# Kernel tuning notes

Measured on AMD Instinct MI355X. Metric: run time of the kernel, lower is better.

Reference implementation:

```python
import jax, jax.numpy as jnp
import numpy as np

TEMPERATURE = 0.01  # clamped min is 0.01, so constant temp stays 0.01
MASK_VAL = -10000.0


def setup_inputs() -> dict:
    key = jax.random.key(0)
    k1, k2 = jax.random.split(key)
    B, C, D = 512, 16, 128
    ts_features = jax.random.normal(k1, (B, C, D), dtype=jnp.float32)
    note_features = jax.random.normal(k2, (B, C, D), dtype=jnp.float32)
    return {"ts_features": ts_features, "note_features": note_features}


def reference(ts_features, note_features):
    B, C, D = ts_features.shape
    N = B * C
    ts = ts_features.reshape(N, D)
    nt = note_features.reshape(N, D)

    # sim[i, j] = <ts_i, nt_j>
    sim = jnp.einsum('id,jd->ij', ts, nt)

    # block-diagonal mask: within each CxC block, off-diagonal -> -10000, diagonal kept
    idx = jnp.arange(N)
    blk = idx // C
    same_block = blk[:, None] == blk[None, :]
    is_diag = idx[:, None] == idx[None, :]
    sim_new = jnp.where(same_block & ~is_diag, jnp.asarray(MASK_VAL, sim.dtype), sim)

    logits = sim_new / TEMPERATURE
    # cross entropy with labels = arange(N), both directions
    lsm_r = jax.nn.log_softmax(logits, axis=-1)
    lsm_c = jax.nn.log_softmax(logits.T, axis=-1)
    diag_ids = (idx, idx)
    ce_r = -jnp.mean(lsm_r[diag_ids])
    ce_c = -jnp.mean(lsm_c[diag_ids])
    total_loss = (ce_r + ce_c) / 2

    # nan/inf -> 0 as in the original
    total_loss = jnp.where(jnp.isnan(total_loss) | jnp.isinf(total_loss),
                           jnp.asarray(0.0, total_loss.dtype), total_loss)
    return total_loss
```

## Files before the change

### kernel.cpp

```cpp
#include <hip/hip_runtime.h>
#include <stdint.h>

#define NROWS 8192
#define DDIM  128
#define PPART 8
#define BROWS 256
#define NITER 32
#define LOG2E_X100 144.26950408889634f
#define LN2F       0.6931471805599453f

typedef __bf16 bf16x8 __attribute__((ext_vector_type(8)));
typedef float  f32x4  __attribute__((ext_vector_type(4)));

__device__ __forceinline__ unsigned short f2bf_rne(float f) {
    union { float f; uint32_t u; } v; v.f = f;
    uint32_t r = (v.u + 0x7FFFu + ((v.u >> 16) & 1u)) >> 16;
    return (unsigned short)r;
}

__device__ __forceinline__ void async16(const unsigned short* g, unsigned char* l) {
    __builtin_amdgcn_global_load_lds(
        (const __attribute__((address_space(1))) unsigned int*)g,
        (__attribute__((address_space(3))) unsigned int*)l, 16, 0, 0);
}

__global__ void convert_kernel(const float* __restrict__ ts, const float* __restrict__ nt,
                               unsigned short* __restrict__ ts_bf,
                               unsigned short* __restrict__ nt_bf,
                               float* __restrict__ acc, int* __restrict__ ticket) {
    const int nvec = (NROWS * DDIM) / 4;
    int tid = blockIdx.x * blockDim.x + threadIdx.x;
    bool isNT = tid >= nvec;
    int i = isNT ? (tid - nvec) : tid;
    const float4 v = ((const float4*)(isNT ? nt : ts))[i];
    float sc = isNT ? 1.0f : LOG2E_X100;
    ushort4 o;
    o.x = f2bf_rne(v.x * sc); o.y = f2bf_rne(v.y * sc);
    o.z = f2bf_rne(v.z * sc); o.w = f2bf_rne(v.w * sc);
    ((ushort4*)(isNT ? nt_bf : ts_bf))[i] = o;
    if (tid == 0) { *acc = 0.0f; *ticket = 0; }
}

__device__ __forceinline__ void dma_pair(const unsigned short* gbase, unsigned char* lds, int lane) {
#pragma unroll
    for (int u = 0; u < 8; ++u) {
        int r  = u * 4 + (lane >> 4);
        int ch = (lane & 15) ^ (r & 7);
        async16(gbase + r * 128 + ch * 8, lds + u * 1024);
    }
}

__global__ __launch_bounds__(512, 4) void rowstats_kernel(
        const unsigned short* __restrict__ ts_bf,
        const unsigned short* __restrict__ nt_bf,
        float* __restrict__ pm, float* __restrict__ ps, float* __restrict__ pd) {
    __shared__ unsigned char smem[2 * 8192];

    const int lane = threadIdx.x & 63;
    const int wv   = threadIdx.x >> 6;
    const int c    = lane & 15;
    const int quad = lane >> 4;
    const int bx   = blockIdx.x;
    const int part = blockIdx.y;
    const int dir  = blockIdx.z;
    const int rows0 = bx * BROWS + wv * 32;

    const unsigned short* A = dir ? nt_bf : ts_bf;
    const unsigned short* B = dir ? ts_bf : nt_bf;

    bf16x8 a[2][4];
#pragma unroll
    for (int s = 0; s < 2; ++s) {
        const unsigned short* abase = A + (rows0 + s * 16 + c) * DDIM + quad * 8;
#pragma unroll
        for (int kc = 0; kc < 4; ++kc)
            a[s][kc] = *(const bf16x8*)(abase + kc * 32);
    }

    float m[2][4], ss[2][4], dg[2][4];
#pragma unroll
    for (int s = 0; s < 2; ++s)
#pragma unroll
        for (int r = 0; r < 4; ++r) { m[r? (r):(r)][0] = m[s][r]; }
#pragma unroll
    for (int s = 0; s < 2; ++s)
#pragma unroll
        for (int r = 0; r < 4; ++r) { m[s][r] = -INFINITY; ss[s][r] = 0.0f; dg[s][r] = 0.0f; }

    const bool havePart = (part == (bx >> 2));
    const int  diag_t   = ((bx & 3) << 3) + wv;

    const unsigned short* bwalk = B + (part * (NROWS / PPART)) * DDIM;

    if (wv == 0) dma_pair(bwalk, smem, lane);
    __syncthreads();

    const int ldsoff0 = c * 256 + (((0 * 4) + quad) ^ (c & 7)) * 16;

    for (int t = 0; t < NITER; ++t) {
        if (wv == 0 && t + 1 < NITER)
            dma_pair(bwalk + (t + 1) * 32 * DDIM, smem + ((t + 1) & 1) * 8192, lane);

        const unsigned char* buf = smem + (t & 1) * 8192;

        f32x4 aA0 = {0,0,0,0}, aA1 = {0,0,0,0}, aB0 = {0,0,0,0}, aB1 = {0,0,0,0};
#pragma unroll
        for (int kc = 0; kc < 4; ++kc) {
            const int sw = ((kc * 4 + quad) ^ (c & 7)) * 16;
            bf16x8 bA = *(const bf16x8*)(buf + c * 256 + sw);
            bf16x8 bB = *(const bf16x8*)(buf + (16 + c) * 256 + sw);
            aA0 = __builtin_amdgcn_mfma_f32_16x16x32_bf16(a[0][kc], bA, aA0, 0, 0, 0);
            aA1 = __builtin_amdgcn_mfma_f32_16x16x32_bf16(a[1][kc], bA, aA1, 0, 0, 0);
            aB0 = __builtin_amdgcn_mfma_f32_16x16x32_bf16(a[0][kc], bB, aB0, 0, 0, 0);
            aB1 = __builtin_amdgcn_mfma_f32_16x16x32_bf16(a[1][kc], bB, aB1, 0, 0, 0);
        }

        const bool pd_ = havePart && (t == diag_t);
#pragma unroll
        for (int s = 0; s < 2; ++s) {
#pragma unroll
            for (int r = 0; r < 4; ++r) {
                float xA = s ? aA1[r] : aA0[r];
                float xB = s ? aB1[r] : aB0[r];
                if (pd_) {
                    bool onDiag = (c == quad * 4 + r);
                    if (s == 0) { if (onDiag) dg[0][r] += xA; xA = onDiag ? xA : -1.0e30f; }
                    else        { if (onDiag) dg[1][r] += xB; xB = onDiag ? xB : -1.0e30f; }
                }
                float mn = fmaxf(fmaxf(m[s][r], xA), xB);
                ss[s][r] = ss[s][r] * __builtin_amdgcn_exp2f(m[s][r] - mn)
                         + __builtin_amdgcn_exp2f(xA - mn)
                         + __builtin_amdgcn_exp2f(xB - mn);
                m[s][r] = mn;
            }
        }
        __syncthreads();
    }

#pragma unroll
    for (int s = 0; s < 2; ++s) {
#pragma unroll
        for (int r = 0; r < 4; ++r) {
            float mm = m[s][r], sv = ss[s][r], dd = dg[s][r];
#pragma unroll
            for (int off = 1; off < 16; off <<= 1) {
                float m2 = __shfl_xor(mm, off, 64);
                float s2 = __shfl_xor(sv, off, 64);
                float d2 = __shfl_xor(dd, off, 64);
                float mn = fmaxf(mm, m2);
                sv = sv * __builtin_amdgcn_exp2f(mm - mn) + s2 * __builtin_amdgcn_exp2f(m2 - mn);
                mm = mn;
                dd += d2;
            }
            if (c == 0) {
                int row = rows0 + s * 16 + quad * 4 + r;
                int idx = (dir * NROWS + row) * PPART + part;
                pm[idx] = mm; ps[idx] = sv; pd[idx] = dd;
            }
        }
    }
}

__global__ void merge_kernel(const float* __restrict__ pm, const float* __restrict__ ps,
                             const float* __restrict__ pd, float* __restrict__ acc,
                             int* __restrict__ ticket, float* __restrict__ out) {
    int tid = blockIdx.x * blockDim.x + threadIdx.x;
    const float* pmr = pm + tid * PPART;
    const float* psr = ps + tid * PPART;
    const float* pdr = pd + tid * PPART;
    float mt = -INFINITY;
#pragma unroll
    for (int p = 0; p < PPART; ++p) mt = fmaxf(mt, pmr[p]);
    float st = 0.0f, dt = 0.0f;
#pragma unroll
    for (int p = 0; p < PPART; ++p) {
        st += psr[p] * __builtin_amdgcn_exp2f(pmr[p] - mt);
        dt += pdr[p];
    }
    float lsm = dt - mt - __builtin_amdgcn_logf(st);

    float v = lsm;
#pragma unroll
    for (int off = 32; off; off >>= 1) v += __shfl_down(v, off, 64);
    __shared__ float wsum[4];
    if ((threadIdx.x & 63) == 0) wsum[threadIdx.x >> 6] = v;
    __syncthreads();
    if (threadIdx.x == 0) {
        atomicAdd(acc, wsum[0] + wsum[1] + wsum[2] + wsum[3]);
        __threadfence();
        int old = atomicAdd(ticket, 1);
        if (old == (int)gridDim.x - 1) {
            __threadfence();
            float tot = atomicAdd(acc, 0.0f);
            float t = -(tot * LN2F) / (2.0f * NROWS);
            if (!isfinite(t)) t = 0.0f;
            out[0] = t;
        }
    }
}

extern "C" void kernel_launch(void* const* d_in, const int* in_sizes, int n_in,
                              void* d_out, int out_size, void* d_ws, size_t ws_size,
                              hipStream_t stream) {
    const float* ts = (const float*)d_in[0];
    const float* nt = (const float*)d_in[1];
    float* out = (float*)d_out;

    unsigned short* ts_bf = (unsigned short*)d_ws;
    unsigned short* nt_bf = ts_bf + NROWS * DDIM;
    float* pm = (float*)(nt_bf + NROWS * DDIM);
    float* ps = pm + 2 * NROWS * PPART;
    float* pd = ps + 2 * NROWS * PPART;
    float* acc = pd + 2 * NROWS * PPART;
    int* ticket = (int*)(acc + 1);

    convert_kernel<<<2048, 256, 0, stream>>>(ts, nt, ts_bf, nt_bf, acc, ticket);
    rowstats_kernel<<<dim3(NROWS / BROWS, PPART, 2), 512, 0, stream>>>(ts_bf, nt_bf, pm, ps, pd);
    merge_kernel<<<(2 * NROWS) / 256, 256, 0, stream>>>(pm, ps, pd, acc, ticket, out);
}
```

Baseline: 117.5 us.

## Widen B tiles to 64 rows, spread DMA over all waves, simplify reductions

Result: faster. 110.0 us (-6.4%).

```diff
diff --git a/kernel.cpp b/kernel.cpp
--- a/kernel.cpp
+++ b/kernel.cpp
@@ -5,7 +5,7 @@
 #define DDIM  128
 #define PPART 8
 #define BROWS 256
-#define NITER 32
+#define NITER 16
 #define LOG2E_X100 144.26950408889634f
 #define LN2F       0.6931471805599453f
 
@@ -41,12 +41,14 @@
     if (tid == 0) { *acc = 0.0f; *ticket = 0; }
 }
 
-__device__ __forceinline__ void dma_pair(const unsigned short* gbase, unsigned char* lds, int lane) {
-#pragma unroll
-    for (int u = 0; u < 8; ++u) {
-        int r  = u * 4 + (lane >> 4);
+__device__ __forceinline__ void dma_stage(const unsigned short* g, unsigned char* l,
+                                          int lane, int wv) {
+#pragma unroll
+    for (int k = 0; k < 2; ++k) {
+        int u = wv * 2 + k;
+        int r = u * 4 + (lane >> 4);
         int ch = (lane & 15) ^ (r & 7);
-        async16(gbase + r * 128 + ch * 8, lds + u * 1024);
+        async16(g + r * 128 + ch * 8, l + u * 1024);
     }
 }
 
@@ -54,7 +56,7 @@
         const unsigned short* __restrict__ ts_bf,
         const unsigned short* __restrict__ nt_bf,
         float* __restrict__ pm, float* __restrict__ ps, float* __restrict__ pd) {
-    __shared__ unsigned char smem[2 * 8192];
+    __shared__ unsigned char smem[2 * 16384];
 
     const int lane = threadIdx.x & 63;
     const int wv   = threadIdx.x >> 6;
@@ -81,56 +83,68 @@
 #pragma unroll
     for (int s = 0; s < 2; ++s)
 #pragma unroll
-        for (int r = 0; r < 4; ++r) { m[r? (r):(r)][0] = m[s][r]; }
-#pragma unroll
-    for (int s = 0; s < 2; ++s)
-#pragma unroll
         for (int r = 0; r < 4; ++r) { m[s][r] = -INFINITY; ss[s][r] = 0.0f; dg[s][r] = 0.0f; }
 
     const bool havePart = (part == (bx >> 2));
-    const int  diag_t   = ((bx & 3) << 3) + wv;
-
-    const unsigned short* bwalk = B + (part * (NROWS / PPART)) * DDIM;
-
-    if (wv == 0) dma_pair(bwalk, smem, lane);
+    const int  t_d = (bx & 3) * 4 + (wv >> 1);
+    const int  l0  = (wv & 1) * 2;
+
+    const unsigned short* bwalk = B + part * (NROWS / PPART) * DDIM;
+
+    dma_stage(bwalk, smem, lane, wv);
     __syncthreads();
 
-    const int ldsoff0 = c * 256 + (((0 * 4) + quad) ^ (c & 7)) * 16;
-
     for (int t = 0; t < NITER; ++t) {
-        if (wv == 0 && t + 1 < NITER)
-            dma_pair(bwalk + (t + 1) * 32 * DDIM, smem + ((t + 1) & 1) * 8192, lane);
-
-        const unsigned char* buf = smem + (t & 1) * 8192;
-
-        f32x4 aA0 = {0,0,0,0}, aA1 = {0,0,0,0}, aB0 = {0,0,0,0}, aB1 = {0,0,0,0};
+        if (t + 1 < NITER)
+            dma_stage(bwalk + (t + 1) * 64 * DDIM, smem + ((t + 1) & 1) * 16384, lane, wv);
+
+        const unsigned char* buf = smem + (t & 1) * 16384;
+
+        f32x4 acc[4][2];
+#pragma unroll
+        for (int l = 0; l < 4; ++l)
+#pragma unroll
+            for (int s = 0; s < 2; ++s) acc[l][s] = (f32x4){0.f, 0.f, 0.f, 0.f};
+
 #pragma unroll
         for (int kc = 0; kc < 4; ++kc) {
             const int sw = ((kc * 4 + quad) ^ (c & 7)) * 16;
-            bf16x8 bA = *(const bf16x8*)(buf + c * 256 + sw);
-            bf16x8 bB = *(const bf16x8*)(buf + (16 + c) * 256 + sw);
-            aA0 = __builtin_amdgcn_mfma_f32_16x16x32_bf16(a[0][kc], bA, aA0, 0, 0, 0);
-            aA1 = __builtin_amdgcn_mfma_f32_16x16x32_bf16(a[1][kc], bA, aA1, 0, 0, 0);
-            aB0 = __builtin_amdgcn_mfma_f32_16x16x32_bf16(a[0][kc], bB, aB0, 0, 0, 0);
-            aB1 = __builtin_amdgcn_mfma_f32_16x16x32_bf16(a[1][kc], bB, aB1, 0, 0, 0);
-        }
-
-        const bool pd_ = havePart && (t == diag_t);
+            const unsigned char* p = buf + c * 256 + sw;
+            bf16x8 b0 = *(const bf16x8*)(p);
+            bf16x8 b1 = *(const bf16x8*)(p + 4096);
+            bf16x8 b2 = *(const bf16x8*)(p + 8192);
+            bf16x8 b3 = *(const bf16x8*)(p + 12288);
+            acc[0][0] = __builtin_amdgcn_mfma_f32_16x16x32_bf16(a[0][kc], b0, acc[0][0], 0, 0, 0);
+            acc[0][1] = __builtin_amdgcn_mfma_f32_16x16x32_bf16(a[1][kc], b0, acc[0][1], 0, 0, 0);
+            acc[1][0] = __builtin_amdgcn_mfma_f32_16x16x32_bf16(a[0][kc], b1, acc[1][0], 0, 0, 0);
+            acc[1][1] = __builtin_amdgcn_mfma_f32_16x16x32_bf16(a[1][kc], b1, acc[1][1], 0, 0, 0);
+            acc[2][0] = __builtin_amdgcn_mfma_f32_16x16x32_bf16(a[0][kc], b2, acc[2][0], 0, 0, 0);
+            acc[2][1] = __builtin_amdgcn_mfma_f32_16x16x32_bf16(a[1][kc], b2, acc[2][1], 0, 0, 0);
+            acc[3][0] = __builtin_amdgcn_mfma_f32_16x16x32_bf16(a[0][kc], b3, acc[3][0], 0, 0, 0);
+            acc[3][1] = __builtin_amdgcn_mfma_f32_16x16x32_bf16(a[1][kc], b3, acc[3][1], 0, 0, 0);
+        }
+
+        const bool pd_ = havePart && (t == t_d);
 #pragma unroll
         for (int s = 0; s < 2; ++s) {
 #pragma unroll
             for (int r = 0; r < 4; ++r) {
-                float xA = s ? aA1[r] : aA0[r];
-                float xB = s ? aB1[r] : aB0[r];
+                float x0 = acc[0][s][r], x1 = acc[1][s][r];
+                float x2 = acc[2][s][r], x3 = acc[3][s][r];
                 if (pd_) {
+                    const int dslot = l0 + s;
                     bool onDiag = (c == quad * 4 + r);
-                    if (s == 0) { if (onDiag) dg[0][r] += xA; xA = onDiag ? xA : -1.0e30f; }
-                    else        { if (onDiag) dg[1][r] += xB; xB = onDiag ? xB : -1.0e30f; }
+                    float xv = dslot == 0 ? x0 : dslot == 1 ? x1 : dslot == 2 ? x2 : x3;
+                    if (onDiag) dg[s][r] += xv;
+                    float rep = onDiag ? xv : -1.0e30f;
+                    if (dslot == 0) x0 = rep; else if (dslot == 1) x1 = rep;
+                    else if (dslot == 2) x2 = rep; else x3 = rep;
                 }
-                float mn = fmaxf(fmaxf(m[s][r], xA), xB);
-                ss[s][r] = ss[s][r] * __builtin_amdgcn_exp2f(m[s][r] - mn)
-                         + __builtin_amdgcn_exp2f(xA - mn)
-                         + __builtin_amdgcn_exp2f(xB - mn);
+                float mn = fmaxf(fmaxf(fmaxf(x0, x1), fmaxf(x2, x3)), m[s][r]);
+                float e  = __builtin_amdgcn_exp2f(m[s][r] - mn);
+                float es = (__builtin_amdgcn_exp2f(x0 - mn) + __builtin_amdgcn_exp2f(x1 - mn))
+                         + (__builtin_amdgcn_exp2f(x2 - mn) + __builtin_amdgcn_exp2f(x3 - mn));
+                ss[s][r] = fmaf(ss[s][r], e, es);
                 m[s][r] = mn;
             }
         }
@@ -141,16 +155,16 @@
     for (int s = 0; s < 2; ++s) {
 #pragma unroll
         for (int r = 0; r < 4; ++r) {
-            float mm = m[s][r], sv = ss[s][r], dd = dg[s][r];
+            float mm = m[s][r];
+#pragma unroll
+            for (int off = 1; off < 16; off <<= 1)
+                mm = fmaxf(mm, __shfl_xor(mm, off, 64));
+            float sv = ss[s][r] * __builtin_amdgcn_exp2f(m[s][r] - mm);
+            float dd = dg[s][r];
 #pragma unroll
             for (int off = 1; off < 16; off <<= 1) {
-                float m2 = __shfl_xor(mm, off, 64);
-                float s2 = __shfl_xor(sv, off, 64);
-                float d2 = __shfl_xor(dd, off, 64);
-                float mn = fmaxf(mm, m2);
-                sv = sv * __builtin_amdgcn_exp2f(mm - mn) + s2 * __builtin_amdgcn_exp2f(m2 - mn);
-                mm = mn;
-                dd += d2;
+                sv += __shfl_xor(sv, off, 64);
+                dd += __shfl_xor(dd, off, 64);
             }
             if (c == 0) {
                 int row = rows0 + s * 16 + quad * 4 + r;
```
